# Optimization experiments

Hardware: AMD Instinct MI355X
Metric: run time of the kernel (lower is better)

Reference implementation:

```python
import math
import jax, jax.numpy as jnp
import numpy as np

NUM_BITS = 8
NUM_CHUNKS = 16
EPS = 1e-5


def quantize_ste(x, mn, mx, num_bits=NUM_BITS):
    """Uniform affine quantize with straight-through estimator (repo's UniformQuantize,
    enforce_true_zero=False). mn/mx are treated as constants (repo casts to float())."""
    mn = jax.lax.stop_gradient(mn)
    mx = jax.lax.stop_gradient(mx)
    qmax = 2.0 ** num_bits - 1.0
    scale = jnp.maximum((mx - mn) / qmax, 1e-8)
    q = jnp.round(jnp.clip((x - mn) / scale, 0.0, qmax)) * scale + mn
    return x + jax.lax.stop_gradient(q - x)


def quant_measure(x):
    """QuantMeasure in training mode: min/max = mean over batch of per-sample min/max."""
    xf = jax.lax.stop_gradient(x.reshape(x.shape[0], -1))
    mn = xf.min(axis=-1).mean()
    mx = xf.max(axis=-1).mean()
    return quantize_ste(x, mn, mx, NUM_BITS)


def qconv2d(x, w, b, stride, padding, groups):
    """QConv2d forward: quantize input (QuantMeasure), weight and bias (per-tensor min/max),
    then standard conv. Grad quantization / biprecision only affects backward numerics."""
    qx = quant_measure(x)
    qw = quantize_ste(w, w.min(), w.max(), NUM_BITS)
    out = jax.lax.conv_general_dilated(
        qx, qw, window_strides=(stride, stride),
        padding=[(padding, padding), (padding, padding)],
        feature_group_count=groups,
        dimension_numbers=('NCHW', 'OIHW', 'NCHW'))
    if b is not None:
        qb = quantize_ste(b, b.min(), b.max(), NUM_BITS)
        out = out + qb[None, :, None, None]
    return out


def range_bn(x, weight, bias):
    """RangeBN (training mode): range-based scale estimate over NUM_CHUNKS chunks."""
    x = quant_measure(x)
    B, C, H, W = x.shape
    y = jnp.transpose(x, (1, 0, 2, 3)).reshape(C, NUM_CHUNKS, -1)  # [C, chunks, BHW/chunks]
    mean_max = y.max(axis=-1).mean(axis=-1)   # [C]
    mean_min = y.min(axis=-1).mean(axis=-1)   # [C]
    mean = y.reshape(C, -1).mean(axis=-1)     # [C]
    n = y.shape[-1]
    scale_fix = (0.5 * 0.35) * (1 + (math.pi * math.log(4)) ** 0.5) / ((2 * math.log(n)) ** 0.5)
    scale = 1.0 / ((mean_max - mean_min) * scale_fix + EPS)
    scale = quantize_ste(scale, scale.min(), scale.max(), NUM_BITS)
    out = (x - mean[None, :, None, None]) * scale[None, :, None, None]
    qw = quantize_ste(weight, weight.min(), weight.max(), NUM_BITS)
    out = out * qw[None, :, None, None]
    out = out + bias[None, :, None, None]
    return out


def setup_inputs() -> dict:
    key = jax.random.key(0)
    ks = jax.random.split(key, 8)
    B, Cin, Cout, H, W, K = 32, 256, 256, 56, 56, 3
    x = jax.random.normal(ks[0], (B, Cin, H, W), dtype=jnp.float32)
    # depthwise conv: groups=Cin -> weight [Cin, 1, K, K], kaiming-ish scale
    dw_w = jax.random.normal(ks[1], (Cin, 1, K, K), dtype=jnp.float32) * (1.0 / K)
    dw_b = jax.random.normal(ks[2], (Cin,), dtype=jnp.float32) * 0.1
    bn1_w = jax.random.uniform(ks[3], (Cin,), dtype=jnp.float32)
    bn1_b = jnp.zeros((Cin,), dtype=jnp.float32)
    # pointwise conv: [Cout, Cin, 1, 1], bias=False
    pw_w = jax.random.normal(ks[4], (Cout, Cin, 1, 1), dtype=jnp.float32) * (1.0 / math.sqrt(Cin))
    bn2_w = jax.random.uniform(ks[5], (Cout,), dtype=jnp.float32)
    bn2_b = jnp.zeros((Cout,), dtype=jnp.float32)
    return {"x": x, "dw_w": dw_w, "dw_b": dw_b, "bn1_w": bn1_w, "bn1_b": bn1_b,
            "pw_w": pw_w, "bn2_w": bn2_w, "bn2_b": bn2_b}


def reference(x, dw_w, dw_b, bn1_w, bn1_b, pw_w, bn2_w, bn2_b):
    Cin = x.shape[1]
    h = qconv2d(x, dw_w, dw_b, stride=1, padding=1, groups=Cin)  # depthwise QConv2d
    h = jax.nn.relu(range_bn(h, bn1_w, bn1_b))
    h = qconv2d(h, pw_w, None, stride=1, padding=0, groups=1)    # pointwise QConv2d (no bias)
    h = jax.nn.relu(range_bn(h, bn2_w, bn2_b))
    return h
```

## Files before the change

### kernel.cpp

```cpp
#include <hip/hip_runtime.h>
#include <math.h>

#define IMG 56
#define HW 3136
#define NCH 256
#define NB 32
#define SAMPLE (NCH*HW)
#define TOT (NB*SAMPLE)

typedef short s16x8 __attribute__((ext_vector_type(8)));
typedef float f32x4 __attribute__((ext_vector_type(4)));


__device__ __forceinline__ float qz(float x, float mn, float scale) {
    float t = (x - mn) / scale;
    t = fminf(fmaxf(t, 0.f), 255.f);
    return rintf(t) * scale + mn;
}

__device__ __forceinline__ float codef(float x, float mn, float scale) {
    return rintf(fminf(fmaxf((x - mn) / scale, 0.f), 255.f));
}

__device__ __forceinline__ unsigned bf16u(float v) {
    return (__float_as_uint(v) >> 16) & 0xFFFFu;
}

__device__ __forceinline__ unsigned enc(float f) {
    unsigned u = __float_as_uint(f);
    return (u & 0x80000000u) ? ~u : (u ^ 0x80000000u);
}
__device__ __forceinline__ float dec(unsigned u) {
    unsigned v = (u & 0x80000000u) ? (u ^ 0x80000000u) : ~u;
    return __uint_as_float(v);
}

__device__ __forceinline__ void blk_red_minmax(float& mn, float& mx) {
    __shared__ float smn[4], smx[4];
    __syncthreads();
    #pragma unroll
    for (int o = 32; o > 0; o >>= 1) {
        mn = fminf(mn, __shfl_down(mn, o));
        mx = fmaxf(mx, __shfl_down(mx, o));
    }
    int lane = threadIdx.x & 63, w = threadIdx.x >> 6;
    if (lane == 0) { smn[w] = mn; smx[w] = mx; }
    __syncthreads();
    if (threadIdx.x == 0) {
        int nw = (int)blockDim.x >> 6;
        for (int i = 1; i < nw; i++) { mn = fminf(mn, smn[i]); mx = fmaxf(mx, smx[i]); }
    }
}

__device__ __forceinline__ void blk_red_minmax_bcast(float& mn, float& mx) {
    __shared__ float bb[2];
    blk_red_minmax(mn, mx);
    if (threadIdx.x == 0) { bb[0] = mn; bb[1] = mx; }
    __syncthreads();
    mn = bb[0]; mx = bb[1];
}

__device__ __forceinline__ float blk_red_sum(float v) {
    __shared__ float ss[4];
    __syncthreads();
    #pragma unroll
    for (int o = 32; o > 0; o >>= 1) v += __shfl_down(v, o);
    int lane = threadIdx.x & 63, w = threadIdx.x >> 6;
    if (lane == 0) ss[w] = v;
    __syncthreads();
    if (threadIdx.x == 0) {
        int nw = (int)blockDim.x >> 6;
        for (int i = 1; i < nw; i++) v += ss[i];
    }
    return v;
}


__global__ void k_init(unsigned* xsl, unsigned* pwsl, unsigned* o2mn, unsigned* o2mx, float* o2sum) {
    int i = blockIdx.x * 256 + threadIdx.x;
    o2mn[i] = 0xFFFFFFFFu; o2mx[i] = 0u; o2sum[i] = 0.f;
    if (blockIdx.x == 0) {
        if (threadIdx.x < 64) xsl[threadIdx.x] = (threadIdx.x < 32) ? 0xFFFFFFFFu : 0u;
        if (threadIdx.x == 64) { pwsl[0] = 0xFFFFFFFFu; pwsl[1] = 0u; }
    }
}

__global__ __launch_bounds__(256) void k_pwmm(const float4* __restrict__ pw4, unsigned* pwsl) {
    int i = blockIdx.x * 256 + threadIdx.x;
    float4 v = pw4[i];
    float mn = fminf(fminf(v.x, v.y), fminf(v.z, v.w));
    float mx = fmaxf(fmaxf(v.x, v.y), fmaxf(v.z, v.w));
    blk_red_minmax(mn, mx);
    if (threadIdx.x == 0) { atomicMin(&pwsl[0], enc(mn)); atomicMax(&pwsl[1], enc(mx)); }
}

__global__ __launch_bounds__(256) void k_minmax_x(const float4* __restrict__ x4, unsigned* xsl) {
    int b = blockIdx.y, blk = blockIdx.x;
    const float4* p = x4 + (size_t)b * 200704 + (size_t)blk * 12544;
    float mn = INFINITY, mx = -INFINITY;
    for (int k = threadIdx.x; k < 12544; k += 256) {
        float4 v = p[k];
        mn = fminf(mn, fminf(fminf(v.x, v.y), fminf(v.z, v.w)));
        mx = fmaxf(mx, fmaxf(fmaxf(v.x, v.y), fmaxf(v.z, v.w)));
    }
    blk_red_minmax(mn, mx);
    if (threadIdx.x == 0) {
        atomicMin(&xsl[b], enc(mn));
        atomicMax(&xsl[32 + b], enc(mx));
    }
}

__global__ void k_fin1(const float* __restrict__ dww, const float* __restrict__ dwb,
                       const unsigned* __restrict__ xsl, float* sc) {
    int tid = threadIdx.x;
    float mn = INFINITY, mx = -INFINITY;
    for (int i = tid; i < 2304; i += 256) { float v = dww[i]; mn = fminf(mn, v); mx = fmaxf(mx, v); }
    blk_red_minmax(mn, mx);
    float w1min = mn, w1max = mx;
    float v = dwb[tid]; mn = v; mx = v;
    blk_red_minmax(mn, mx);
    if (tid == 0) {
        float sm = 0.f, sx = 0.f;
        for (int i = 0; i < 32; i++) { sm += dec(xsl[i]); sx += dec(xsl[32 + i]); }
        float m = sm / 32.f, X = sx / 32.f;
        sc[0] = m;      sc[1] = fmaxf((X - m) / 255.f, 1e-8f);
        sc[2] = w1min;  sc[3] = fmaxf((w1max - w1min) / 255.f, 1e-8f);
        sc[4] = mn;     sc[5] = fmaxf((mx - mn) / 255.f, 1e-8f);
    }
}

__global__ __launch_bounds__(256) void k_dwconv(const float4* __restrict__ x4, const float* __restrict__ w,
                                                const float* __restrict__ bias, float* __restrict__ h1,
                                                const float* __restrict__ sc,
                                                float* __restrict__ h1mn, float* __restrict__ h1mx,
                                                float* __restrict__ h1sm) {
    int bc = blockIdx.x, c = bc & 255;
    __shared__ float tile[58 * 68];
    int tid = threadIdx.x;
    for (int i = tid; i < 58 * 68; i += 256) tile[i] = 0.f;
    __syncthreads();
    float mnx = sc[0], scx = sc[1];
    const float4* px = x4 + (size_t)bc * 784;
    #pragma unroll
    for (int it = 0; it < 4; it++) {
        int idx = it * 256 + tid;
        if (idx < 784) {
            int i = idx / 14, j = (idx - i * 14) * 4;
            float4 v = px[idx];
            v.x = qz(v.x, mnx, scx); v.y = qz(v.y, mnx, scx);
            v.z = qz(v.z, mnx, scx); v.w = qz(v.w, mnx, scx);
            *(float4*)&tile[(i + 1) * 68 + j + 4] = v;
        }
    }
    __syncthreads();
    float qw[9];
    #pragma unroll
    for (int k = 0; k < 9; k++) qw[k] = qz(w[c * 9 + k], sc[2], sc[3]);
    float qb = qz(bias[c], sc[4], sc[5]);
    float4* po = (float4*)(h1 + (size_t)bc * HW);
    float lmn = INFINITY, lmx = -INFINITY, lsum = 0.f;
    #pragma unroll
    for (int it = 0; it < 4; it++) {
        int idx = it * 256 + tid;
        if (idx < 784) {
            int i = idx / 14, j = (idx - i * 14) * 4;
            float o0 = qb, o1 = qb, o2v = qb, o3 = qb;
            #pragma unroll
            for (int r = 0; r < 3; r++) {
                const float* row = &tile[(i + r) * 68 + j + 3];
                float a0 = row[0];
                float4 mid = *(const float4*)&row[1];
                float a5 = row[5];
                float w0 = qw[3 * r], w1 = qw[3 * r + 1], w2 = qw[3 * r + 2];
                o0  += a0    * w0 + mid.x * w1 + mid.y * w2;
                o1  += mid.x * w0 + mid.y * w1 + mid.z * w2;
                o2v += mid.y * w0 + mid.z * w1 + mid.w * w2;
                o3  += mid.z * w0 + mid.w * w1 + a5    * w2;
            }
            po[idx] = make_float4(o0, o1, o2v, o3);
            lmn = fminf(lmn, fminf(fminf(o0, o1), fminf(o2v, o3)));
            lmx = fmaxf(lmx, fmaxf(fmaxf(o0, o1), fmaxf(o2v, o3)));
            lsum += (o0 + o1) + (o2v + o3);
        }
    }
    blk_red_minmax(lmn, lmx);
    float ls = blk_red_sum(lsum);
    if (tid == 0) { h1mn[bc] = lmn; h1mx[bc] = lmx; h1sm[bc] = ls; }
}

__global__ __launch_bounds__(256) void k_stats1(const float* __restrict__ h1mn, const float* __restrict__ h1mx,
                                                const float* __restrict__ h1sm,
                                                const float* __restrict__ bn1w, const float* __restrict__ bn1b,
                                                const unsigned* __restrict__ pwsl, float* sc,
                                                float* __restrict__ P1, float* __restrict__ Q1) {
    int tid = threadIdx.x;
    __shared__ float sp[2];
    float amn = 0.f, amx = 0.f;
    for (int b = 0; b < 32; b++) {
        float mn = h1mn[b * 256 + tid], mx = h1mx[b * 256 + tid];
        blk_red_minmax(mn, mx);
        if (tid == 0) { amn += mn; amx += mx; }
    }
    if (tid == 0) {
        float m = amn / 32.f, X = amx / 32.f;
        sp[0] = m; sp[1] = fmaxf((X - m) / 255.f, 1e-8f);
        sc[6] = sp[0]; sc[7] = sp[1];
    }
    __syncthreads();
    float mn1 = sp[0], s1 = sp[1];
    int c = tid;
    float mmax = 0.f, mmin = 0.f, sum = 0.f;
    for (int ck = 0; ck < 16; ck++) {
        float c0n = h1mn[(2 * ck) * 256 + c], c1n = h1mn[(2 * ck + 1) * 256 + c];
        float c0x = h1mx[(2 * ck) * 256 + c], c1x = h1mx[(2 * ck + 1) * 256 + c];
        mmin += qz(fminf(c0n, c1n), mn1, s1);
        mmax += qz(fmaxf(c0x, c1x), mn1, s1);
        sum  += h1sm[(2 * ck) * 256 + c] + h1sm[(2 * ck + 1) * 256 + c];
    }
    mmin *= 0.0625f; mmax *= 0.0625f;
    float mean = sum / 100352.f;
    const float scale_fix = (float)(0.175 * (1.0 + sqrt(3.14159265358979323846 * log(4.0))) / sqrt(2.0 * log(6272.0)));
    float scale = 1.f / ((mmax - mmin) * scale_fix + 1e-5f);
    float ssn = scale, ssx = scale;
    blk_red_minmax_bcast(ssn, ssx);
    float w = bn1w[c];
    float wmn = w, wmx = w;
    blk_red_minmax_bcast(wmn, wmx);
    float qs = qz(scale, ssn, fmaxf((ssx - ssn) / 255.f, 1e-8f));
    float qw = qz(w, wmn, fmaxf((wmx - wmn) / 255.f, 1e-8f));
    float a1 = qs * qw;
    float be = bn1b[c] - mean * a1;
    float p1v = s1 * a1, q1v = mn1 * a1 + be;
    P1[c] = p1v; Q1[c] = q1v;
    float a2mn = 0.f, a2mx = 0.f;
    for (int b = 0; b < 32; b++) {
        float vn = h1mn[b * 256 + c], vx = h1mx[b * 256 + c];
        float hn = fmaxf(rintf(fminf(fmaxf((vn - mn1) / s1, 0.f), 255.f)) * p1v + q1v, 0.f);
        float hx = fmaxf(rintf(fminf(fmaxf((vx - mn1) / s1, 0.f), 255.f)) * p1v + q1v, 0.f);
        blk_red_minmax(hn, hx);
        if (tid == 0) { a2mn += hn; a2mx += hx; }
    }
    if (tid == 0) {
        float m = a2mn / 32.f, X = a2mx / 32.f;
        sc[8] = m; sc[9] = fmaxf((X - m) / 255.f, 1e-8f);
        float pmn = dec(pwsl[0]), pmx = dec(pwsl[1]);
        sc[10] = pmn; sc[11] = fmaxf((pmx - pmn) / 255.f, 1e-8f);
    }
}

__global__ __launch_bounds__(256) void k_qw(const float* __restrict__ pw, const float* __restrict__ sc,
                                            short* __restrict__ wcodes, float* __restrict__ Wsum) {
    int co = blockIdx.x, ci = threadIdx.x;
    float kw = codef(pw[co * 256 + ci], sc[10], sc[11]);
    wcodes[co * 256 + ci] = (short)bf16u(kw);
    float s = blk_red_sum(kw);
    if (ci == 0) Wsum[co] = s;
}

__global__ __launch_bounds__(256) void k_gemm(const float* __restrict__ h1, const short* __restrict__ wcodes,
                                              const float* __restrict__ Wsum, const float* __restrict__ sc,
                                              const float* __restrict__ P1, const float* __restrict__ Q1,
                                              float* __restrict__ o2,
                                              unsigned* o2mn, unsigned* o2mx, float* o2sum) {
    int b = blockIdx.y, p0 = blockIdx.x * 64;
    __shared__ unsigned AsU[64][20];
    __shared__ float BpP[16][64];
    __shared__ float BpT[64];
    int tid = threadIdx.x, lane = tid & 63, w = tid >> 6;
    int col = lane & 15, quad = lane >> 4;
    int c2 = tid >> 4, pq = tid & 15;
    float mn1 = sc[6], s1 = sc[7], mn2 = sc[8], s2 = sc[9];
    f32x4 acc[4][4];
    #pragma unroll
    for (int i = 0; i < 4; i++)
        #pragma unroll
        for (int j = 0; j < 4; j++) acc[i][j] = (f32x4){0.f, 0.f, 0.f, 0.f};
    float bp[4] = {0.f, 0.f, 0.f, 0.f};
    const float* arow = h1 + ((size_t)b * 256 + 2 * c2) * HW + p0 + pq * 4;
    const short* wbase = wcodes + ((size_t)(w * 64 + col)) * 256 + quad * 8;
    float4 v0 = *(const float4*)arow;
    float4 v1 = *(const float4*)(arow + HW);
    for (int k0 = 0; k0 < 256; k0 += 32) {
        float p1a = P1[k0 + 2 * c2], q1a = Q1[k0 + 2 * c2];
        float p1b = P1[k0 + 2 * c2 + 1], q1b = Q1[k0 + 2 * c2 + 1];
        unsigned pk[4];
        #pragma unroll
        for (int j = 0; j < 4; j++) {
            float va = (&v0.x)[j], vb = (&v1.x)[j];
            float k1a = rintf(fminf(fmaxf((va - mn1) / s1, 0.f), 255.f));
            float h2a = fmaxf(k1a * p1a + q1a, 0.f);
            float ka  = rintf(fminf(fmaxf((h2a - mn2) / s2, 0.f), 255.f));
            float k1b = rintf(fminf(fmaxf((vb - mn1) / s1, 0.f), 255.f));
            float h2b = fmaxf(k1b * p1b + q1b, 0.f);
            float kb  = rintf(fminf(fmaxf((h2b - mn2) / s2, 0.f), 255.f));
            bp[j] += ka + kb;
            pk[j] = bf16u(ka) | (bf16u(kb) << 16);
        }
        __syncthreads();
        #pragma unroll
        for (int j = 0; j < 4; j++) AsU[pq * 4 + j][c2] = pk[j];
        __syncthreads();
        if (k0 + 32 < 256) {
            v0 = *(const float4*)(arow + (size_t)(k0 + 32) * HW);
            v1 = *(const float4*)(arow + (size_t)(k0 + 33) * HW);
        }
        s16x8 af[4], bfr[4];
        #pragma unroll
        for (int mt = 0; mt < 4; mt++) af[mt] = *(const s16x8*)&AsU[mt * 16 + col][quad * 4];
        #pragma unroll
        for (int nt = 0; nt < 4; nt++) bfr[nt] = *(const s16x8*)&wbase[(size_t)nt * 16 * 256 + k0];
        #pragma unroll
        for (int mt = 0; mt < 4; mt++)
            #pragma unroll
            for (int nt = 0; nt < 4; nt++)
                acc[mt][nt] = __builtin_amdgcn_mfma_f32_16x16x32_bf16(af[mt], bfr[nt], acc[mt][nt], 0, 0, 0);
    }
    #pragma unroll
    for (int j = 0; j < 4; j++) BpP[c2][pq * 4 + j] = bp[j];
    __syncthreads();
    if (tid < 64) {
        float s = 0.f;
        #pragma unroll
        for (int i = 0; i < 16; i++) s += BpP[i][tid];
        BpT[tid] = s;
    }
    __syncthreads();
    float alpha = sc[11] * sc[9];
    float beta  = sc[11] * sc[8];
    float gamma = sc[10] * sc[9];
    float delta = 256.f * sc[10] * sc[8];
    float Wv[4];
    #pragma unroll
    for (int nt = 0; nt < 4; nt++) Wv[nt] = Wsum[w * 64 + nt * 16 + col];
    float snn[4], sxx[4], ssm[4];
    #pragma unroll
    for (int nt = 0; nt < 4; nt++) { snn[nt] = INFINITY; sxx[nt] = -INFINITY; ssm[nt] = 0.f; }
    float* obase = o2 + ((size_t)b * HW + p0) * 256 + w * 64 + col;
    #pragma unroll
    for (int mt = 0; mt < 4; mt++) {
        float bp4[4];
        #pragma unroll
        for (int r = 0; r < 4; r++) bp4[r] = BpT[mt * 16 + quad * 4 + r];
        #pragma unroll
        for (int nt = 0; nt < 4; nt++) {
            float wterm = beta * Wv[nt] + delta;
            #pragma unroll
            for (int r = 0; r < 4; r++) {
                float val = alpha * acc[mt][nt][r] + gamma * bp4[r] + wterm;
                obase[(size_t)(mt * 16 + quad * 4 + r) * 256 + nt * 16] = val;
                snn[nt] = fminf(snn[nt], val);
                sxx[nt] = fmaxf(sxx[nt], val);
                ssm[nt] += val;
            }
        }
    }
    #pragma unroll
    for (int nt = 0; nt < 4; nt++) {
        snn[nt] = fminf(snn[nt], __shfl_xor(snn[nt], 16));
        sxx[nt] = fmaxf(sxx[nt], __shfl_xor(sxx[nt], 16));
        ssm[nt] += __shfl_xor(ssm[nt], 16);
        snn[nt] = fminf(snn[nt], __shfl_xor(snn[nt], 32));
        sxx[nt] = fmaxf(sxx[nt], __shfl_xor(sxx[nt], 32));
        ssm[nt] += __shfl_xor(ssm[nt], 32);
    }
    if (lane < 16) {
        #pragma unroll
        for (int nt = 0; nt < 4; nt++) {
            int idx = b * 256 + w * 64 + nt * 16 + lane;
            atomicMin(&o2mn[idx], enc(snn[nt]));
            atomicMax(&o2mx[idx], enc(sxx[nt]));
            atomicAdd(&o2sum[idx], ssm[nt]);
        }
    }
}

__global__ __launch_bounds__(256) void k_stats2(const unsigned* __restrict__ o2mnU, const unsigned* __restrict__ o2mxU,
                                                const float* __restrict__ o2sm,
                                                const float* __restrict__ bn2w, const float* __restrict__ bn2b,
                                                float* sc, float* __restrict__ P2, float* __restrict__ Q2) {
    int tid = threadIdx.x;
    __shared__ float sp[2];
    float amn = 0.f, amx = 0.f;
    for (int b = 0; b < 32; b++) {
        float mn = dec(o2mnU[b * 256 + tid]), mx = dec(o2mxU[b * 256 + tid]);
        blk_red_minmax(mn, mx);
        if (tid == 0) { amn += mn; amx += mx; }
    }
    if (tid == 0) {
        float m = amn / 32.f, X = amx / 32.f;
        sp[0] = m; sp[1] = fmaxf((X - m) / 255.f, 1e-8f);
        sc[12] = sp[0]; sc[13] = sp[1];
    }
    __syncthreads();
    float mno = sp[0], so = sp[1];
    int c = tid;
    float mmax = 0.f, mmin = 0.f, sum = 0.f;
    for (int ck = 0; ck < 16; ck++) {
        float c0n = dec(o2mnU[(2 * ck) * 256 + c]), c1n = dec(o2mnU[(2 * ck + 1) * 256 + c]);
        float c0x = dec(o2mxU[(2 * ck) * 256 + c]), c1x = dec(o2mxU[(2 * ck + 1) * 256 + c]);
        mmin += qz(fminf(c0n, c1n), mno, so);
        mmax += qz(fmaxf(c0x, c1x), mno, so);
        sum  += o2sm[(2 * ck) * 256 + c] + o2sm[(2 * ck + 1) * 256 + c];
    }
    mmin *= 0.0625f; mmax *= 0.0625f;
    float mean = sum / 100352.f;
    const float scale_fix = (float)(0.175 * (1.0 + sqrt(3.14159265358979323846 * log(4.0))) / sqrt(2.0 * log(6272.0)));
    float scale = 1.f / ((mmax - mmin) * scale_fix + 1e-5f);
    float ssn = scale, ssx = scale;
    blk_red_minmax_bcast(ssn, ssx);
    float w = bn2w[c];
    float wmn = w, wmx = w;
    blk_red_minmax_bcast(wmn, wmx);
    float qs = qz(scale, ssn, fmaxf((ssx - ssn) / 255.f, 1e-8f));
    float qw = qz(w, wmn, fmaxf((wmx - wmn) / 255.f, 1e-8f));
    float a2 = qs * qw;
    float be = bn2b[c] - mean * a2;
    P2[c] = so * a2; Q2[c] = mno * a2 + be;
}

__global__ __launch_bounds__(256) void k_apply(const float* __restrict__ o2, const float* __restrict__ sc,
                                               const float* __restrict__ P2, const float* __restrict__ Q2,
                                               float* __restrict__ out) {
    __shared__ float tile[64][65];
    int b = blockIdx.z, p0 = blockIdx.x * 64, co0 = blockIdx.y * 64;
    int t = threadIdx.x, rr = t >> 4, cq = t & 15;
    float mno = sc[12], so = sc[13];
    #pragma unroll
    for (int it = 0; it < 4; it++) {
        int p = rr + 16 * it;
        float4 v = *(const float4*)&o2[((size_t)b * HW + p0 + p) * 256 + co0 + cq * 4];
        *(float4*)&tile[p][cq * 4] = v;
    }
    __syncthreads();
    #pragma unroll
    for (int it = 0; it < 4; it++) {
        int col = rr + 16 * it;
        int c = co0 + col;
        float pv = P2[c], qv = Q2[c];
        float4 r;
        #pragma unroll
        for (int j = 0; j < 4; j++) {
            float val = tile[cq * 4 + j][col];
            (&r.x)[j] = fmaxf(rintf(fminf(fmaxf((val - mno) / so, 0.f), 255.f)) * pv + qv, 0.f);
        }
        *(float4*)&out[((size_t)b * 256 + c) * HW + p0 + cq * 4] = r;
    }
}


extern "C" void kernel_launch(void* const* d_in, const int* in_sizes, int n_in,
                              void* d_out, int out_size, void* d_ws, size_t ws_size,
                              hipStream_t stream) {
    (void)in_sizes; (void)n_in; (void)out_size; (void)ws_size;
    const float* x    = (const float*)d_in[0];
    const float* dww  = (const float*)d_in[1];
    const float* dwb  = (const float*)d_in[2];
    const float* bn1w = (const float*)d_in[3];
    const float* bn1b = (const float*)d_in[4];
    const float* pww  = (const float*)d_in[5];
    const float* bn2w = (const float*)d_in[6];
    const float* bn2b = (const float*)d_in[7];

    float* h1   = (float*)d_ws;
    float* o2   = h1 + TOT;
    float* after = o2 + TOT;
    short* wcodes = (short*)after;
    float* Wsum  = after + 32768;
    float* sc    = Wsum + 256;
    unsigned* xsl   = (unsigned*)(sc + 32);
    unsigned* pwsl  = xsl + 64;
    unsigned* o2mnU = pwsl + 64;
    unsigned* o2mxU = o2mnU + 8192;
    float* o2sm = (float*)(o2mxU + 8192);
    float* h1mn = o2sm + 8192;
    float* h1mx = h1mn + 8192;
    float* h1sm = h1mx + 8192;
    float* P1 = h1sm + 8192; float* Q1 = P1 + 256;
    float* P2 = Q1 + 256;    float* Q2 = P2 + 256;

    k_init<<<32, 256, 0, stream>>>(xsl, pwsl, o2mnU, o2mxU, o2sm);
    k_pwmm<<<64, 256, 0, stream>>>((const float4*)pww, pwsl);
    k_minmax_x<<<dim3(16, 32), 256, 0, stream>>>((const float4*)x, xsl);
    k_fin1<<<1, 256, 0, stream>>>(dww, dwb, xsl, sc);
    k_dwconv<<<NB * NCH, 256, 0, stream>>>((const float4*)x, dww, dwb, h1, sc, h1mn, h1mx, h1sm);
    k_stats1<<<1, 256, 0, stream>>>(h1mn, h1mx, h1sm, bn1w, bn1b, pwsl, sc, P1, Q1);
    k_qw<<<256, 256, 0, stream>>>(pww, sc, wcodes, Wsum);
    k_gemm<<<dim3(49, 32), 256, 0, stream>>>(h1, wcodes, Wsum, sc, P1, Q1, o2, o2mnU, o2mxU, o2sm);
    k_stats2<<<1, 256, 0, stream>>>(o2mnU, o2mxU, o2sm, bn2w, bn2b, sc, P2, Q2);
    k_apply<<<dim3(49, 4, 32), 256, 0, stream>>>(o2, sc, P2, Q2, (float*)d_out);
}
```

Baseline: 440.0 us.

## Stage full K activation tile once in GEMM and fold quantize affine constants

```diff
diff --git a/kernel.cpp b/kernel.cpp
--- a/kernel.cpp
+++ b/kernel.cpp
@@ -7,6 +7,7 @@
 #define NB 32
 #define SAMPLE (NCH*HW)
 #define TOT (NB*SAMPLE)
+#define ASTR 132
 
 typedef short s16x8 __attribute__((ext_vector_type(8)));
 typedef float f32x4 __attribute__((ext_vector_type(4)));
@@ -192,19 +193,32 @@
                                                 const float* __restrict__ h1sm,
                                                 const float* __restrict__ bn1w, const float* __restrict__ bn1b,
                                                 const unsigned* __restrict__ pwsl, float* sc,
-                                                float* __restrict__ P1, float* __restrict__ Q1) {
-    int tid = threadIdx.x;
-    __shared__ float sp[2];
-    float amn = 0.f, amx = 0.f;
-    for (int b = 0; b < 32; b++) {
-        float mn = h1mn[b * 256 + tid], mx = h1mx[b * 256 + tid];
-        blk_red_minmax(mn, mx);
-        if (tid == 0) { amn += mn; amx += mx; }
-    }
+                                                float* __restrict__ P1, float* __restrict__ Q1,
+                                                float* __restrict__ A2v, float* __restrict__ B2v) {
+    int tid = threadIdx.x, lane = tid & 63, w = tid >> 6;
+    __shared__ float bmn[32], bmx[32], sp[4], lP[256], lQ[256];
+    #pragma unroll
+    for (int i = 0; i < 8; i++) {
+        int b = w * 8 + i;
+        float4 m4 = *(const float4*)&h1mn[b * 256 + lane * 4];
+        float4 x4 = *(const float4*)&h1mx[b * 256 + lane * 4];
+        float mn = fminf(fminf(m4.x, m4.y), fminf(m4.z, m4.w));
+        float mx = fmaxf(fmaxf(x4.x, x4.y), fmaxf(x4.z, x4.w));
+        #pragma unroll
+        for (int o = 32; o > 0; o >>= 1) { mn = fminf(mn, __shfl_down(mn, o)); mx = fmaxf(mx, __shfl_down(mx, o)); }
+        if (lane == 0) { bmn[b] = mn; bmx[b] = mx; }
+    }
+    __syncthreads();
     if (tid == 0) {
-        float m = amn / 32.f, X = amx / 32.f;
+        float sm = 0.f, sx = 0.f;
+        for (int i = 0; i < 32; i++) { sm += bmn[i]; sx += bmx[i]; }
+        float m = sm / 32.f, X = sx / 32.f;
         sp[0] = m; sp[1] = fmaxf((X - m) / 255.f, 1e-8f);
         sc[6] = sp[0]; sc[7] = sp[1];
+        sc[14] = 1.f / sp[1];
+        sc[15] = -sp[0] / sp[1];
+        float pmn = dec(pwsl[0]), pmx = dec(pwsl[1]);
+        sc[10] = pmn; sc[11] = fmaxf((pmx - pmn) / 255.f, 1e-8f);
     }
     __syncthreads();
     float mn1 = sp[0], s1 = sp[1];
@@ -223,29 +237,46 @@
     float scale = 1.f / ((mmax - mmin) * scale_fix + 1e-5f);
     float ssn = scale, ssx = scale;
     blk_red_minmax_bcast(ssn, ssx);
-    float w = bn1w[c];
-    float wmn = w, wmx = w;
+    float wv = bn1w[c];
+    float wmn = wv, wmx = wv;
     blk_red_minmax_bcast(wmn, wmx);
     float qs = qz(scale, ssn, fmaxf((ssx - ssn) / 255.f, 1e-8f));
-    float qw = qz(w, wmn, fmaxf((wmx - wmn) / 255.f, 1e-8f));
+    float qw = qz(wv, wmn, fmaxf((wmx - wmn) / 255.f, 1e-8f));
     float a1 = qs * qw;
     float be = bn1b[c] - mean * a1;
     float p1v = s1 * a1, q1v = mn1 * a1 + be;
-    P1[c] = p1v; Q1[c] = q1v;
-    float a2mn = 0.f, a2mx = 0.f;
-    for (int b = 0; b < 32; b++) {
-        float vn = h1mn[b * 256 + c], vx = h1mx[b * 256 + c];
-        float hn = fmaxf(rintf(fminf(fmaxf((vn - mn1) / s1, 0.f), 255.f)) * p1v + q1v, 0.f);
-        float hx = fmaxf(rintf(fminf(fmaxf((vx - mn1) / s1, 0.f), 255.f)) * p1v + q1v, 0.f);
-        blk_red_minmax(hn, hx);
-        if (tid == 0) { a2mn += hn; a2mx += hx; }
-    }
+    P1[c] = p1v; Q1[c] = q1v; lP[c] = p1v; lQ[c] = q1v;
+    __syncthreads();
+    #pragma unroll
+    for (int i = 0; i < 8; i++) {
+        int b = w * 8 + i;
+        float4 m4 = *(const float4*)&h1mn[b * 256 + lane * 4];
+        float4 x4 = *(const float4*)&h1mx[b * 256 + lane * 4];
+        float mn = INFINITY, mx = -INFINITY;
+        #pragma unroll
+        for (int j = 0; j < 4; j++) {
+            int cc = lane * 4 + j;
+            float kn = rintf(fminf(fmaxf(((&m4.x)[j] - mn1) / s1, 0.f), 255.f));
+            float kx = rintf(fminf(fmaxf(((&x4.x)[j] - mn1) / s1, 0.f), 255.f));
+            float hn = fmaxf(kn * lP[cc] + lQ[cc], 0.f);
+            float hx = fmaxf(kx * lP[cc] + lQ[cc], 0.f);
+            mn = fminf(mn, hn); mx = fmaxf(mx, hx);
+        }
+        #pragma unroll
+        for (int o = 32; o > 0; o >>= 1) { mn = fminf(mn, __shfl_down(mn, o)); mx = fmaxf(mx, __shfl_down(mx, o)); }
+        if (lane == 0) { bmn[b] = mn; bmx[b] = mx; }
+    }
+    __syncthreads();
     if (tid == 0) {
-        float m = a2mn / 32.f, X = a2mx / 32.f;
-        sc[8] = m; sc[9] = fmaxf((X - m) / 255.f, 1e-8f);
-        float pmn = dec(pwsl[0]), pmx = dec(pwsl[1]);
-        sc[10] = pmn; sc[11] = fmaxf((pmx - pmn) / 255.f, 1e-8f);
-    }
+        float sm = 0.f, sx = 0.f;
+        for (int i = 0; i < 32; i++) { sm += bmn[i]; sx += bmx[i]; }
+        float m = sm / 32.f, X = sx / 32.f;
+        sp[2] = m; sp[3] = fmaxf((X - m) / 255.f, 1e-8f);
+        sc[8] = sp[2]; sc[9] = sp[3];
+    }
+    __syncthreads();
+    A2v[c] = lP[c] / sp[3];
+    B2v[c] = (lQ[c] - sp[2]) / sp[3];
 }
 
 __global__ __launch_bounds__(256) void k_qw(const float* __restrict__ pw, const float* __restrict__ sc,
@@ -259,71 +290,72 @@
 
 __global__ __launch_bounds__(256) void k_gemm(const float* __restrict__ h1, const short* __restrict__ wcodes,
                                               const float* __restrict__ Wsum, const float* __restrict__ sc,
-                                              const float* __restrict__ P1, const float* __restrict__ Q1,
+                                              const float* __restrict__ A2v, const float* __restrict__ B2v,
                                               float* __restrict__ o2,
                                               unsigned* o2mn, unsigned* o2mx, float* o2sum) {
     int b = blockIdx.y, p0 = blockIdx.x * 64;
-    __shared__ unsigned AsU[64][20];
-    __shared__ float BpP[16][64];
+    __shared__ unsigned AsU[64 * ASTR];
+    __shared__ float BpW[4][64];
     __shared__ float BpT[64];
     int tid = threadIdx.x, lane = tid & 63, w = tid >> 6;
     int col = lane & 15, quad = lane >> 4;
-    int c2 = tid >> 4, pq = tid & 15;
-    float mn1 = sc[6], s1 = sc[7], mn2 = sc[8], s2 = sc[9];
+    float A1 = sc[14], B1 = sc[15];
+    const float* colp = h1 + (size_t)b * SAMPLE + p0 + lane;
+    unsigned base = lane * ASTR + 32 * w;
+    float bp = 0.f;
+    for (int t2 = 0; t2 < 16; t2++) {
+        int d0 = 2 * t2;
+        int ci = 64 * w + 2 * d0;
+        float v0 = colp[(size_t)ci * HW];
+        float v1 = colp[(size_t)(ci + 1) * HW];
+        float v2 = colp[(size_t)(ci + 2) * HW];
+        float v3 = colp[(size_t)(ci + 3) * HW];
+        float k0f = rintf(fminf(fmaxf(fmaf(v0, A1, B1), 0.f), 255.f));
+        float k1f = rintf(fminf(fmaxf(fmaf(v1, A1, B1), 0.f), 255.f));
+        float k2f = rintf(fminf(fmaxf(fmaf(v2, A1, B1), 0.f), 255.f));
+        float k3f = rintf(fminf(fmaxf(fmaf(v3, A1, B1), 0.f), 255.f));
+        float c0 = rintf(fminf(fmaxf(fmaf(k0f, A2v[ci],     B2v[ci]),     0.f), 255.f));
+        float c1 = rintf(fminf(fmaxf(fmaf(k1f, A2v[ci + 1], B2v[ci + 1]), 0.f), 255.f));
+        float c2 = rintf(fminf(fmaxf(fmaf(k2f, A2v[ci + 2], B2v[ci + 2]), 0.f), 255.f));
+        float c3 = rintf(fminf(fmaxf(fmaf(k3f, A2v[ci + 3], B2v[ci + 3]), 0.f), 255.f));
+        bp += (c0 + c1) + (c2 + c3);
+        uint2 pk;
+        pk.x = bf16u(c0) | (bf16u(c1) << 16);
+        pk.y = bf16u(c2) | (bf16u(c3) << 16);
+        *(uint2*)&AsU[base + d0] = pk;
+    }
+    BpW[w][lane] = bp;
+    __syncthreads();
+    const short* wb = wcodes + (size_t)(w * 64 + col) * 256 + quad * 8;
     f32x4 acc[4][4];
     #pragma unroll
     for (int i = 0; i < 4; i++)
         #pragma unroll
         for (int j = 0; j < 4; j++) acc[i][j] = (f32x4){0.f, 0.f, 0.f, 0.f};
-    float bp[4] = {0.f, 0.f, 0.f, 0.f};
-    const float* arow = h1 + ((size_t)b * 256 + 2 * c2) * HW + p0 + pq * 4;
-    const short* wbase = wcodes + ((size_t)(w * 64 + col)) * 256 + quad * 8;
-    float4 v0 = *(const float4*)arow;
-    float4 v1 = *(const float4*)(arow + HW);
-    for (int k0 = 0; k0 < 256; k0 += 32) {
-        float p1a = P1[k0 + 2 * c2], q1a = Q1[k0 + 2 * c2];
-        float p1b = P1[k0 + 2 * c2 + 1], q1b = Q1[k0 + 2 * c2 + 1];
-        unsigned pk[4];
-        #pragma unroll
-        for (int j = 0; j < 4; j++) {
-            float va = (&v0.x)[j], vb = (&v1.x)[j];
-            float k1a = rintf(fminf(fmaxf((va - mn1) / s1, 0.f), 255.f));
-            float h2a = fmaxf(k1a * p1a + q1a, 0.f);
-            float ka  = rintf(fminf(fmaxf((h2a - mn2) / s2, 0.f), 255.f));
-            float k1b = rintf(fminf(fmaxf((vb - mn1) / s1, 0.f), 255.f));
-            float h2b = fmaxf(k1b * p1b + q1b, 0.f);
-            float kb  = rintf(fminf(fmaxf((h2b - mn2) / s2, 0.f), 255.f));
-            bp[j] += ka + kb;
-            pk[j] = bf16u(ka) | (bf16u(kb) << 16);
-        }
-        __syncthreads();
-        #pragma unroll
-        for (int j = 0; j < 4; j++) AsU[pq * 4 + j][c2] = pk[j];
-        __syncthreads();
-        if (k0 + 32 < 256) {
-            v0 = *(const float4*)(arow + (size_t)(k0 + 32) * HW);
-            v1 = *(const float4*)(arow + (size_t)(k0 + 33) * HW);
-        }
-        s16x8 af[4], bfr[4];
-        #pragma unroll
-        for (int mt = 0; mt < 4; mt++) af[mt] = *(const s16x8*)&AsU[mt * 16 + col][quad * 4];
-        #pragma unroll
-        for (int nt = 0; nt < 4; nt++) bfr[nt] = *(const s16x8*)&wbase[(size_t)nt * 16 * 256 + k0];
+    s16x8 bcur[4];
+    #pragma unroll
+    for (int nt = 0; nt < 4; nt++) bcur[nt] = *(const s16x8*)(wb + (size_t)nt * 4096);
+    for (int step = 0; step < 8; step++) {
+        s16x8 af[4];
+        #pragma unroll
+        for (int mt = 0; mt < 4; mt++)
+            af[mt] = *(const s16x8*)&AsU[(size_t)(mt * 16 + col) * ASTR + step * 16 + quad * 4];
+        s16x8 bnx[4];
+        if (step < 7) {
+            #pragma unroll
+            for (int nt = 0; nt < 4; nt++) bnx[nt] = *(const s16x8*)(wb + (size_t)nt * 4096 + (step + 1) * 32);
+        }
         #pragma unroll
         for (int mt = 0; mt < 4; mt++)
             #pragma unroll
             for (int nt = 0; nt < 4; nt++)
-                acc[mt][nt] = __builtin_amdgcn_mfma_f32_16x16x32_bf16(af[mt], bfr[nt], acc[mt][nt], 0, 0, 0);
-    }
-    #pragma unroll
-    for (int j = 0; j < 4; j++) BpP[c2][pq * 4 + j] = bp[j];
-    __syncthreads();
-    if (tid < 64) {
-        float s = 0.f;
-        #pragma unroll
-        for (int i = 0; i < 16; i++) s += BpP[i][tid];
-        BpT[tid] = s;
-    }
+                acc[mt][nt] = __builtin_amdgcn_mfma_f32_16x16x32_bf16(af[mt], bcur[nt], acc[mt][nt], 0, 0, 0);
+        if (step < 7) {
+            #pragma unroll
+            for (int nt = 0; nt < 4; nt++) bcur[nt] = bnx[nt];
+        }
+    }
+    if (tid < 64) BpT[tid] = BpW[0][tid] + BpW[1][tid] + BpW[2][tid] + BpW[3][tid];
     __syncthreads();
     float alpha = sc[11] * sc[9];
     float beta  = sc[11] * sc[8];
@@ -378,16 +410,24 @@
                                                 const float* __restrict__ o2sm,
                                                 const float* __restrict__ bn2w, const float* __restrict__ bn2b,
                                                 float* sc, float* __restrict__ P2, float* __restrict__ Q2) {
-    int tid = threadIdx.x;
-    __shared__ float sp[2];
-    float amn = 0.f, amx = 0.f;
-    for (int b = 0; b < 32; b++) {
-        float mn = dec(o2mnU[b * 256 + tid]), mx = dec(o2mxU[b * 256 + tid]);
-        blk_red_minmax(mn, mx);
-        if (tid == 0) { amn += mn; amx += mx; }
-    }
+    int tid = threadIdx.x, lane = tid & 63, w = tid >> 6;
+    __shared__ float bmn[32], bmx[32], sp[2];
+    #pragma unroll
+    for (int i = 0; i < 8; i++) {
+        int b = w * 8 + i;
+        uint4 um = *(const uint4*)&o2mnU[b * 256 + lane * 4];
+        uint4 ux = *(const uint4*)&o2mxU[b * 256 + lane * 4];
+        float mn = fminf(fminf(dec(um.x), dec(um.y)), fminf(dec(um.z), dec(um.w)));
+        float mx = fmaxf(fmaxf(dec(ux.x), dec(ux.y)), fmaxf(dec(ux.z), dec(ux.w)));
+        #pragma unroll
+        for (int o = 32; o > 0; o >>= 1) { mn = fminf(mn, __shfl_down(mn, o)); mx = fmaxf(mx, __shfl_down(mx, o)); }
+        if (lane == 0) { bmn[b] = mn; bmx[b] = mx; }
+    }
+    __syncthreads();
     if (tid == 0) {
-        float m = amn / 32.f, X = amx / 32.f;
+        float sm = 0.f, sx = 0.f;
+        for (int i = 0; i < 32; i++) { sm += bmn[i]; sx += bmx[i]; }
+        float m = sm / 32.f, X = sx / 32.f;
         sp[0] = m; sp[1] = fmaxf((X - m) / 255.f, 1e-8f);
         sc[12] = sp[0]; sc[13] = sp[1];
     }
@@ -408,11 +448,11 @@
     float scale = 1.f / ((mmax - mmin) * scale_fix + 1e-5f);
     float ssn = scale, ssx = scale;
     blk_red_minmax_bcast(ssn, ssx);
-    float w = bn2w[c];
-    float wmn = w, wmx = w;
+    float wv = bn2w[c];
+    float wmn = wv, wmx = wv;
     blk_red_minmax_bcast(wmn, wmx);
     float qs = qz(scale, ssn, fmaxf((ssx - ssn) / 255.f, 1e-8f));
-    float qw = qz(w, wmn, fmaxf((wmx - wmn) / 255.f, 1e-8f));
+    float qw = qz(wv, wmn, fmaxf((wmx - wmn) / 255.f, 1e-8f));
     float a2 = qs * qw;
     float be = bn2b[c] - mean * a2;
     P2[c] = so * a2; Q2[c] = mno * a2 + be;
@@ -477,15 +517,16 @@
     float* h1sm = h1mx + 8192;
     float* P1 = h1sm + 8192; float* Q1 = P1 + 256;
     float* P2 = Q1 + 256;    float* Q2 = P2 + 256;
+    float* A2v = Q2 + 256;   float* B2v = A2v + 256;
 
     k_init<<<32, 256, 0, stream>>>(xsl, pwsl, o2mnU, o2mxU, o2sm);
     k_pwmm<<<64, 256, 0, stream>>>((const float4*)pww, pwsl);
     k_minmax_x<<<dim3(16, 32), 256, 0, stream>>>((const float4*)x, xsl);
     k_fin1<<<1, 256, 0, stream>>>(dww, dwb, xsl, sc);
     k_dwconv<<<NB * NCH, 256, 0, stream>>>((const float4*)x, dww, dwb, h1, sc, h1mn, h1mx, h1sm);
-    k_stats1<<<1, 256, 0, stream>>>(h1mn, h1mx, h1sm, bn1w, bn1b, pwsl, sc, P1, Q1);
+    k_stats1<<<1, 256, 0, stream>>>(h1mn, h1mx, h1sm, bn1w, bn1b, pwsl, sc, P1, Q1, A2v, B2v);
     k_qw<<<256, 256, 0, stream>>>(pww, sc, wcodes, Wsum);
-    k_gemm<<<dim3(49, 32), 256, 0, stream>>>(h1, wcodes, Wsum, sc, P1, Q1, o2, o2mnU, o2mxU, o2sm);
+    k_gemm<<<dim3(49, 32), 256, 0, stream>>>(h1, wcodes, Wsum, sc, A2v, B2v, o2, o2mnU, o2mxU, o2sm);
     k_stats2<<<1, 256, 0, stream>>>(o2mnU, o2mxU, o2sm, bn2w, bn2b, sc, P2, Q2);
     k_apply<<<dim3(49, 4, 32), 256, 0, stream>>>(o2, sc, P2, Q2, (float*)d_out);
 }
```

Measured after the change: 385.3 us. -12.4%, faster.
